# Optimization experiments

Hardware: AMD Instinct MI355X
Metric: run time of the kernel (lower is better)

The kernel has to match this reference:

```python
import jax, jax.numpy as jnp
import numpy as np

B, H, E = 32768, 1024, 512
VOCAB = 1600 * 20  # input_dim * 20


def setup_inputs() -> dict:
    key = jax.random.key(0)
    ks = jax.random.split(key, 13)
    sc_e = 1.0 / np.sqrt(E)
    sc_h = 1.0 / np.sqrt(H)
    sc_2h = 1.0 / np.sqrt(2 * H)
    # weights stored as [in, out] (transpose of torch Linear.weight)
    return {
        "s_t_minus_1": jax.random.normal(ks[0], (B, 1, H), jnp.float32),
        "y_t_minus_1": jax.random.randint(ks[1], (B, 1), 0, VOCAB, jnp.int64 if jax.config.jax_enable_x64 else jnp.int32),
        "c_t": jax.random.normal(ks[2], (B, 1, 2 * H), jnp.float32),
        "emb": jax.random.normal(ks[3], (VOCAB, E), jnp.float32),
        "Wz": jax.random.uniform(ks[4], (E, H), jnp.float32, -sc_e, sc_e),
        "Uz": jax.random.uniform(ks[5], (H, H), jnp.float32, -sc_h, sc_h),
        "Cz": jax.random.uniform(ks[6], (2 * H, H), jnp.float32, -sc_2h, sc_2h),
        "Wr": jax.random.uniform(ks[7], (E, H), jnp.float32, -sc_e, sc_e),
        "Ur": jax.random.uniform(ks[8], (H, H), jnp.float32, -sc_h, sc_h),
        "Cr": jax.random.uniform(ks[9], (2 * H, H), jnp.float32, -sc_2h, sc_2h),
        "W": jax.random.uniform(ks[10], (E, H), jnp.float32, -sc_e, sc_e),
        "U": jax.random.uniform(ks[11], (H, H), jnp.float32, -sc_h, sc_h),
        "C": jax.random.uniform(ks[12], (2 * H, H), jnp.float32, -sc_2h, sc_2h),
    }


def reference(s_t_minus_1, y_t_minus_1, c_t, emb, Wz, Uz, Cz, Wr, Ur, Cr, W, U, C):
    # embedding lookup: (B,1) -> (B,1,E)
    y = emb[y_t_minus_1]
    # gates, all contractions over last axis
    z_t = jax.nn.sigmoid(y @ Wz + s_t_minus_1 @ Uz + c_t @ Cz)  # (B,1,H)
    r_t = jax.nn.sigmoid(y @ Wr + s_t_minus_1 @ Ur + c_t @ Cr)  # (B,1,H)
    s_tilde = jnp.tanh(y @ W + (r_t * s_t_minus_1) @ U + c_t @ C)
    s_t = (1.0 - z_t) * s_t_minus_1 + z_t * s_tilde
    return s_t
```

## Files before the change

kernel.cpp:

```cpp
#include <hip/hip_runtime.h>

typedef unsigned short u16;
typedef float  f32x4  __attribute__((ext_vector_type(4)));
typedef short  bf16x8 __attribute__((ext_vector_type(8)));
typedef u16    u16x8  __attribute__((ext_vector_type(8)));

#define BROWS 32768
#define KTOT  3584
#define NKT   (KTOT / 64)

static __device__ __forceinline__ u16 f2b(float f) {
    unsigned x = __float_as_uint(f);
    x += 0x7fffu + ((x >> 16) & 1u);
    return (u16)(x >> 16);
}
static __device__ __forceinline__ float b2f(u16 u) {
    return __uint_as_float(((unsigned)u) << 16);
}
static __device__ __forceinline__ float sigm(float x) {
    return 1.f / (1.f + __expf(-x));
}
static __device__ __forceinline__ float tanh_s(float x) {
    float ax = fabsf(x);
    float e  = __expf(-2.f * ax);
    float t  = (1.f - e) / (1.f + e);
    return copysignf(t, x);
}
static __device__ __forceinline__ void gld16(const u16* g, u16* l) {
    __builtin_amdgcn_global_load_lds(
        (const __attribute__((address_space(1))) void*)g,
        (__attribute__((address_space(3))) void*)l, 16, 0, 0);
}

__global__ __launch_bounds__(256) void pack_x(
    const float* __restrict__ s, const int* __restrict__ y,
    const float* __restrict__ c, const float* __restrict__ emb,
    u16* __restrict__ X)
{
    long tid = (long)blockIdx.x * 256 + threadIdx.x;
    int  row = (int)(tid / 448);
    int  seg = (int)(tid % 448);
    int  e0  = seg * 8;
    const float* src;
    if (e0 < 512)        src = emb + (long)y[row] * 512 + e0;
    else if (e0 < 1536)  src = s   + (long)row * 1024 + (e0 - 512);
    else                 src = c   + (long)row * 2048 + (e0 - 1536);
    f32x4 a = *(const f32x4*)src;
    f32x4 b = *(const f32x4*)(src + 4);
    u16x8 o;
    o[0]=f2b(a[0]); o[1]=f2b(a[1]); o[2]=f2b(a[2]); o[3]=f2b(a[3]);
    o[4]=f2b(b[0]); o[5]=f2b(b[1]); o[6]=f2b(b[2]); o[7]=f2b(b[3]);
    *(u16x8*)&X[(long)row * KTOT + e0] = o;
}

__global__ __launch_bounds__(256) void wtrans_all(
    const float* __restrict__ Wz, const float* __restrict__ Uz,
    const float* __restrict__ Cz, const float* __restrict__ Wr,
    const float* __restrict__ Ur, const float* __restrict__ Cr,
    const float* __restrict__ W,  const float* __restrict__ U,
    const float* __restrict__ C,
    u16* __restrict__ WzrT, u16* __restrict__ W2T)
{
    __shared__ float t[32][33];
    int z = blockIdx.z;
    const float* src; u16* dst; int kd;
    switch (z) {
        case 0: src = Wz; dst = WzrT + 0;                  kd = 512;  break;
        case 1: src = Uz; dst = WzrT + 512;                kd = 1024; break;
        case 2: src = Cz; dst = WzrT + 1536;               kd = 2048; break;
        case 3: src = Wr; dst = WzrT + 1024 * KTOT;        kd = 512;  break;
        case 4: src = Ur; dst = WzrT + 1024 * KTOT + 512;  kd = 1024; break;
        case 5: src = Cr; dst = WzrT + 1024 * KTOT + 1536; kd = 2048; break;
        case 6: src = W;  dst = W2T + 0;                   kd = 512;  break;
        case 7: src = U;  dst = W2T + 512;                 kd = 1024; break;
        default: src = C; dst = W2T + 1536;                kd = 2048; break;
    }
    int k0 = blockIdx.x * 32;
    if (k0 >= kd) return;
    int n0 = blockIdx.y * 32;
    int tx = threadIdx.x, ty = threadIdx.y;
    #pragma unroll
    for (int r = ty; r < 32; r += 8)
        t[r][tx] = src[(long)(k0 + r) * 1024 + n0 + tx];
    __syncthreads();
    #pragma unroll
    for (int r = ty; r < 32; r += 8)
        dst[(long)(n0 + r) * KTOT + k0 + tx] = f2b(t[tx][r]);
}


#define RDA(P,m,ks)  a[m][ks]  = *(const bf16x8*)((P) + (m)*1024 + (ks)*512 + lane_off)
#define RDB(P,n,ks)  bb[n][ks] = *(const bf16x8*)((P) + (n)*1024 + (ks)*512 + lane_off)
#define RDA4(P,m0)   RDA(P,m0,0);RDA(P,m0,1);RDA(P,m0+1,0);RDA(P,m0+1,1);RDA(P,m0+2,0);RDA(P,m0+2,1);RDA(P,m0+3,0);RDA(P,m0+3,1)
#define RDB2(P,n0)   RDB(P,n0,0);RDB(P,n0,1);RDB(P,n0+1,0);RDB(P,n0+1,1)
#define MM1(m,n,ks) acc[m][n] = __builtin_amdgcn_mfma_f32_16x16x32_bf16(a[m][ks], bb[n][ks], acc[m][n], 0, 0, 0)
#define MMROW(m,n0) MM1(m,n0,0); MM1(m,n0,1); MM1(m,n0+1,0); MM1(m,n0+1,1)
#define MMQUAD(m0,n0) MMROW(m0,n0); MMROW(m0+1,n0); MMROW(m0+2,n0); MMROW(m0+3,n0)

#define PH_MID \
    __builtin_amdgcn_s_barrier(); \
    asm volatile("s_waitcnt lgkmcnt(0)" ::: "memory"); \
    __builtin_amdgcn_sched_barrier(0); \
    __builtin_amdgcn_s_setprio(1);

#define PH_END \
    __builtin_amdgcn_s_setprio(0); \
    __builtin_amdgcn_sched_barrier(0); \
    __builtin_amdgcn_s_barrier();

template<int MODE>
__global__ __launch_bounds__(512, 1) void gemm8(
    const u16* __restrict__ Xc, const u16* __restrict__ rsin,
    const u16* __restrict__ Wt,
    u16* __restrict__ zb, u16* __restrict__ rsb,
    const u16* __restrict__ zread, float* __restrict__ out, int NT)
{
    extern __shared__ u16 smem[];

    int bid = blockIdx.x, nwg = gridDim.x;
    int q   = nwg >> 3;
    int wg  = (bid & 7) * q + (bid >> 3);
    int bm  = wg / NT, bn = wg % NT;
    int R0  = bm * 256;
    int C0  = bn * 256;

    int t = threadIdx.x, w = t >> 6, l = t & 63;
    int wr = w >> 2, wc = w & 3;

    int rl   = l >> 2;
    int ccl  = ((l & 3) * 8) ^ ((l >> 5) * 16);
    int sr0  = w >> 1, sc = w & 1;
    int colb = sc * 32 + ccl;
    int offAx[2][2], offAr[2][2], offB[2][2];
    #pragma unroll
    for (int h = 0; h < 2; h++)
        #pragma unroll
        for (int i = 0; i < 2; i++) {
            int row = h * 128 + (sr0 + i * 4) * 16 + rl;
            offAx[h][i] = (R0 + row) * KTOT + colb;
            offAr[h][i] = (R0 + row) * 1024 + colb - 512;
            offB [h][i] = (C0 + row) * KTOT + colb;
        }

    auto stageA = [&](int kt) {
        int k0 = kt * 64;
        u16* Ld = smem + (kt & 1) * 32768;
        bool useR = (MODE == 1) && (k0 >= 512) && (k0 < 1536);
        #pragma unroll
        for (int h = 0; h < 2; h++)
            #pragma unroll
            for (int i = 0; i < 2; i++) {
                const u16* g = useR ? (rsin + (offAr[h][i] + k0))
                                    : (Xc   + (offAx[h][i] + k0));
                gld16(g, Ld + h * 8192 + (w + i * 8) * 512);
            }
    };
    auto stageB = [&](int kt) {
        int k0 = kt * 64;
        u16* Ld = smem + (kt & 1) * 32768 + 16384;
        #pragma unroll
        for (int h = 0; h < 2; h++)
            #pragma unroll
            for (int i = 0; i < 2; i++)
                gld16(Wt + (offB[h][i] + k0),
                      Ld + h * 8192 + (w + i * 8) * 512);
    };

    int lane_off = (l & 15) * 32 + (((l >> 4) * 8) ^ (((l >> 3) & 1) * 16));

    f32x4 acc[8][4];
    #pragma unroll
    for (int m = 0; m < 8; m++)
        #pragma unroll
        for (int n = 0; n < 4; n++)
            acc[m][n] = (f32x4){0.f, 0.f, 0.f, 0.f};

    bf16x8 a[8][2], bb[4][2];

    int aoff = wr * 8192;
    int boff = 16384 + (wc >> 1) * 8192 + (wc & 1) * 4096;

    stageA(0); stageB(0);
    stageA(1); stageB(1);
    asm volatile("s_waitcnt vmcnt(8)" ::: "memory");
    __builtin_amdgcn_s_barrier();
    {
        const u16* A0 = smem + aoff;
        const u16* B0 = smem + boff;
        RDA4(A0, 0); RDB2(B0, 0);
    }

    for (int kt = 0; kt < NKT; ++kt) {
        int bs = kt & 1;
        const u16* Ab = smem + bs * 32768 + aoff;
        const u16* Bb = smem + bs * 32768 + boff;
        const u16* An = smem + (bs ^ 1) * 32768 + aoff;
        const u16* Bn = smem + (bs ^ 1) * 32768 + boff;

        PH_MID; MMQUAD(0, 0); RDB2(Bb, 2); PH_END;
        PH_MID; MMQUAD(0, 2); RDA4(Ab, 4); PH_END;
        if (kt + 2 < NKT) stageB(kt + 2);
        PH_MID; MMQUAD(4, 2); PH_END;
        if (kt + 2 < NKT) {
            stageA(kt + 2);
            asm volatile("s_waitcnt vmcnt(8)" ::: "memory");
        } else {
            asm volatile("s_waitcnt vmcnt(0)" ::: "memory");
        }
        PH_MID; MMQUAD(4, 0);
        if (kt + 1 < NKT) { RDA4(An, 0); RDB2(Bn, 0); }
        PH_END;
    }

    int lr = (l >> 4) * 4, lc = l & 15;
    long R0w = R0 + wr * 128;
    int  C0w = C0 + wc * 64;
    if (MODE == 0) {
        if (C0 < 1024) {
            #pragma unroll
            for (int m = 0; m < 8; m++)
                #pragma unroll
                for (int n = 0; n < 4; n++) {
                    int col = C0w + n * 16 + lc;
                    #pragma unroll
                    for (int j = 0; j < 4; j++) {
                        long r = R0w + m * 16 + lr + j;
                        zb[r * 1024 + col] = f2b(sigm(acc[m][n][j]));
                    }
                }
        } else {
            #pragma unroll
            for (int m = 0; m < 8; m++)
                #pragma unroll
                for (int n = 0; n < 4; n++) {
                    int h = C0w + n * 16 + lc - 1024;
                    #pragma unroll
                    for (int j = 0; j < 4; j++) {
                        long r = R0w + m * 16 + lr + j;
                        float sv = b2f(Xc[r * KTOT + 512 + h]);
                        float rr = sigm(acc[m][n][j]);
                        rsb[r * 1024 + h] = f2b(rr * sv);
                    }
                }
        }
    } else {
        #pragma unroll
        for (int m = 0; m < 8; m++)
            #pragma unroll
            for (int n = 0; n < 4; n++) {
                int col = C0w + n * 16 + lc;
                #pragma unroll
                for (int j = 0; j < 4; j++) {
                    long r = R0w + m * 16 + lr + j;
                    float st = tanh_s(acc[m][n][j]);
                    float z  = b2f(zread[r * 1024 + col]);
                    float sv = b2f(Xc[r * KTOT + 512 + col]);
                    out[r * 1024 + col] = fmaf(z, st - sv, sv);
                }
            }
    }
}

extern "C" void kernel_launch(void* const* d_in, const int* in_sizes, int n_in,
                              void* d_out, int out_size, void* d_ws, size_t ws_size,
                              hipStream_t stream)
{
    const float* s   = (const float*)d_in[0];
    const int*   y   = (const int*)  d_in[1];
    const float* c   = (const float*)d_in[2];
    const float* emb = (const float*)d_in[3];
    const float* Wz  = (const float*)d_in[4];
    const float* Uz  = (const float*)d_in[5];
    const float* Cz  = (const float*)d_in[6];
    const float* Wr  = (const float*)d_in[7];
    const float* Ur  = (const float*)d_in[8];
    const float* Cr  = (const float*)d_in[9];
    const float* W   = (const float*)d_in[10];
    const float* U   = (const float*)d_in[11];
    const float* C   = (const float*)d_in[12];
    float* out = (float*)d_out;

    char* ws = (char*)d_ws;
    u16* Xcat = (u16*)(ws);
    u16* rsb  = (u16*)(ws + 234881024);
    u16* zbuf = (u16*)(ws + 301989888);
    u16* WzrT = (u16*)(ws + 369098752);
    u16* W2T  = (u16*)(ws + 383778816);

    hipFuncSetAttribute((const void*)gemm8<0>,
                        hipFuncAttributeMaxDynamicSharedMemorySize, 131072);
    hipFuncSetAttribute((const void*)gemm8<1>,
                        hipFuncAttributeMaxDynamicSharedMemorySize, 131072);

    pack_x<<<BROWS * 448 / 256, 256, 0, stream>>>(s, y, c, emb, Xcat);

    dim3 tb(32, 8);
    wtrans_all<<<dim3(64, 32, 9), tb, 0, stream>>>(
        Wz, Uz, Cz, Wr, Ur, Cr, W, U, C, WzrT, W2T);

    gemm8<0><<<(BROWS / 256) * (2048 / 256), 512, 131072, stream>>>(
        Xcat, nullptr, WzrT, zbuf, rsb, nullptr, nullptr, 2048 / 256);

    gemm8<1><<<(BROWS / 256) * (1024 / 256), 512, 131072, stream>>>(
        Xcat, rsb, W2T, nullptr, nullptr, zbuf, out, 1024 / 256);
}
```

Before: 803.8 us.

## Switch GEMM inner loop from 16x16x32 to 32x32x16 bf16 MFMA tiles

Replaces the 16x16x32 MFMA instruction with the 32x32x16 variant, reorganising the per-wave accumulators into 4x2 tiles of 32x32. LDS fragment reads and lane offsets are remapped to the new operand layout, and the epilogue indexing follows the 32x32 output layout. Larger MFMA tiles issue fewer instructions and fewer LDS reads per FLOP, which lowers LDS bandwidth pressure. The cost is a different register footprint and possible LDS bank conflicts with the existing swizzle.

```diff
diff --git a/kernel.cpp b/kernel.cpp
--- a/kernel.cpp
+++ b/kernel.cpp
@@ -1,9 +1,10 @@
 #include <hip/hip_runtime.h>
 
 typedef unsigned short u16;
-typedef float  f32x4  __attribute__((ext_vector_type(4)));
-typedef short  bf16x8 __attribute__((ext_vector_type(8)));
-typedef u16    u16x8  __attribute__((ext_vector_type(8)));
+typedef float  f32x4   __attribute__((ext_vector_type(4)));
+typedef float  f32x16  __attribute__((ext_vector_type(16)));
+typedef short  bf16x8  __attribute__((ext_vector_type(8)));
+typedef u16    u16x8   __attribute__((ext_vector_type(8)));
 
 #define BROWS 32768
 #define KTOT  3584
@@ -89,13 +90,14 @@
 }
 
 
-#define RDA(P,m,ks)  a[m][ks]  = *(const bf16x8*)((P) + (m)*1024 + (ks)*512 + lane_off)
-#define RDB(P,n,ks)  bb[n][ks] = *(const bf16x8*)((P) + (n)*1024 + (ks)*512 + lane_off)
-#define RDA4(P,m0)   RDA(P,m0,0);RDA(P,m0,1);RDA(P,m0+1,0);RDA(P,m0+1,1);RDA(P,m0+2,0);RDA(P,m0+2,1);RDA(P,m0+3,0);RDA(P,m0+3,1)
-#define RDB2(P,n0)   RDB(P,n0,0);RDB(P,n0,1);RDB(P,n0+1,0);RDB(P,n0+1,1)
-#define MM1(m,n,ks) acc[m][n] = __builtin_amdgcn_mfma_f32_16x16x32_bf16(a[m][ks], bb[n][ks], acc[m][n], 0, 0, 0)
-#define MMROW(m,n0) MM1(m,n0,0); MM1(m,n0,1); MM1(m,n0+1,0); MM1(m,n0+1,1)
-#define MMQUAD(m0,n0) MMROW(m0,n0); MMROW(m0+1,n0); MMROW(m0+2,n0); MMROW(m0+3,n0)
+#define RDA32(P,mt,ks) a[mt][ks] = *(const bf16x8*)((P) + (mt)*2048 + ((ks)>>1)*512 + (((ks)&1) ? laneX : laneO))
+#define RDB32(P,nt,ks) b[nt][ks] = *(const bf16x8*)((P) + (nt)*2048 + ((ks)>>1)*512 + (((ks)&1) ? laneX : laneO))
+#define RDA_T(P,mt) RDA32(P,mt,0); RDA32(P,mt,1); RDA32(P,mt,2); RDA32(P,mt,3)
+#define RDB_T(P,nt) RDB32(P,nt,0); RDB32(P,nt,1); RDB32(P,nt,2); RDB32(P,nt,3)
+#define MM32(mt,nt,ks) acc[mt][nt] = __builtin_amdgcn_mfma_f32_32x32x16_bf16(a[mt][ks], b[nt][ks], acc[mt][nt], 0, 0, 0)
+#define MMQ32(m0,m1,nt) \
+    MM32(m0,nt,0); MM32(m1,nt,0); MM32(m0,nt,1); MM32(m1,nt,1); \
+    MM32(m0,nt,2); MM32(m1,nt,2); MM32(m0,nt,3); MM32(m1,nt,3)
 
 #define PH_MID \
     __builtin_amdgcn_s_barrier(); \
@@ -166,29 +168,31 @@
                       Ld + h * 8192 + (w + i * 8) * 512);
     };
 
-    int lane_off = (l & 15) * 32 + (((l >> 4) * 8) ^ (((l >> 3) & 1) * 16));
-
-    f32x4 acc[8][4];
+    int laneO = ((l >> 4) & 1) * 1024 + (l & 15) * 32
+              + (((l >> 5) * 8) ^ (((l >> 3) & 1) * 16));
+    int laneX = laneO ^ 16;
+
+    f32x16 acc[4][2];
     #pragma unroll
-    for (int m = 0; m < 8; m++)
-        #pragma unroll
-        for (int n = 0; n < 4; n++)
-            acc[m][n] = (f32x4){0.f, 0.f, 0.f, 0.f};
-
-    bf16x8 a[8][2], bb[4][2];
+    for (int mt = 0; mt < 4; mt++)
+        #pragma unroll
+        for (int nt = 0; nt < 2; nt++)
+            acc[mt][nt] = (f32x16)(0.f);
+
+    bf16x8 a[4][4], b[2][4];
 
     int aoff = wr * 8192;
-    int boff = 16384 + (wc >> 1) * 8192 + (wc & 1) * 4096;
+    int boff = 16384 + wc * 4096;
+    const u16* Ae = smem + aoff;
+    const u16* Be = smem + boff;
+    const u16* Ao = Ae + 32768;
+    const u16* Bo = Be + 32768;
 
     stageA(0); stageB(0);
     stageA(1); stageB(1);
     asm volatile("s_waitcnt vmcnt(8)" ::: "memory");
     __builtin_amdgcn_s_barrier();
-    {
-        const u16* A0 = smem + aoff;
-        const u16* B0 = smem + boff;
-        RDA4(A0, 0); RDB2(B0, 0);
-    }
+    RDA_T(Ae, 0); RDA_T(Ae, 1); RDB_T(Be, 0);
 
     for (int kt = 0; kt < NKT; ++kt) {
         int bs = kt & 1;
@@ -197,66 +201,72 @@
         const u16* An = smem + (bs ^ 1) * 32768 + aoff;
         const u16* Bn = smem + (bs ^ 1) * 32768 + boff;
 
-        PH_MID; MMQUAD(0, 0); RDB2(Bb, 2); PH_END;
-        PH_MID; MMQUAD(0, 2); RDA4(Ab, 4); PH_END;
+        PH_MID; MMQ32(0, 1, 0); RDB_T(Bb, 1); PH_END;
+        PH_MID; MMQ32(0, 1, 1); RDA_T(Ab, 2); RDA_T(Ab, 3); PH_END;
         if (kt + 2 < NKT) stageB(kt + 2);
-        PH_MID; MMQUAD(4, 2); PH_END;
+        PH_MID; MMQ32(2, 3, 1); PH_END;
         if (kt + 2 < NKT) {
             stageA(kt + 2);
             asm volatile("s_waitcnt vmcnt(8)" ::: "memory");
         } else {
             asm volatile("s_waitcnt vmcnt(0)" ::: "memory");
         }
-        PH_MID; MMQUAD(4, 0);
-        if (kt + 1 < NKT) { RDA4(An, 0); RDB2(Bn, 0); }
+        PH_MID; MMQ32(2, 3, 0);
+        if (kt + 1 < NKT) { RDA_T(An, 0); RDA_T(An, 1); RDB_T(Bn, 0); }
         PH_END;
     }
 
-    int lr = (l >> 4) * 4, lc = l & 15;
+    int hi4 = (l >> 5) * 4, lc32 = l & 31;
     long R0w = R0 + wr * 128;
     int  C0w = C0 + wc * 64;
     if (MODE == 0) {
         if (C0 < 1024) {
             #pragma unroll
-            for (int m = 0; m < 8; m++)
+            for (int mt = 0; mt < 4; mt++)
                 #pragma unroll
-                for (int n = 0; n < 4; n++) {
-                    int col = C0w + n * 16 + lc;
+                for (int nt = 0; nt < 2; nt++) {
+                    int col = C0w + nt * 32 + lc32;
                     #pragma unroll
-                    for (int j = 0; j < 4; j++) {
-                        long r = R0w + m * 16 + lr + j;
-                        zb[r * 1024 + col] = f2b(sigm(acc[m][n][j]));
-                    }
+                    for (int qq = 0; qq < 4; qq++)
+                        #pragma unroll
+                        for (int jj = 0; jj < 4; jj++) {
+                            long r = R0w + mt * 32 + qq * 8 + hi4 + jj;
+                            zb[r * 1024 + col] = f2b(sigm(acc[mt][nt][qq * 4 + jj]));
+                        }
                 }
         } else {
             #pragma unroll
-            for (int m = 0; m < 8; m++)
+            for (int mt = 0; mt < 4; mt++)
                 #pragma unroll
-                for (int n = 0; n < 4; n++) {
-                    int h = C0w + n * 16 + lc - 1024;
+                for (int nt = 0; nt < 2; nt++) {
+                    int h = C0w + nt * 32 + lc32 - 1024;
                     #pragma unroll
-                    for (int j = 0; j < 4; j++) {
-                        long r = R0w + m * 16 + lr + j;
-                        float sv = b2f(Xc[r * KTOT + 512 + h]);
-                        float rr = sigm(acc[m][n][j]);
-                        rsb[r * 1024 + h] = f2b(rr * sv);
-                    }
+                    for (int qq = 0; qq < 4; qq++)
+                        #pragma unroll
+                        for (int jj = 0; jj < 4; jj++) {
+                            long r = R0w + mt * 32 + qq * 8 + hi4 + jj;
+                            float sv = b2f(Xc[r * KTOT + 512 + h]);
+                            float rr = sigm(acc[mt][nt][qq * 4 + jj]);
+                            rsb[r * 1024 + h] = f2b(rr * sv);
+                        }
                 }
         }
     } else {
         #pragma unroll
-        for (int m = 0; m < 8; m++)
-            #pragma unroll
-            for (int n = 0; n < 4; n++) {
-                int col = C0w + n * 16 + lc;
+        for (int mt = 0; mt < 4; mt++)
+            #pragma unroll
+            for (int nt = 0; nt < 2; nt++) {
+                int col = C0w + nt * 32 + lc32;
                 #pragma unroll
-                for (int j = 0; j < 4; j++) {
-                    long r = R0w + m * 16 + lr + j;
-                    float st = tanh_s(acc[m][n][j]);
-                    float z  = b2f(zread[r * 1024 + col]);
-                    float sv = b2f(Xc[r * KTOT + 512 + col]);
-                    out[r * 1024 + col] = fmaf(z, st - sv, sv);
-                }
+                for (int qq = 0; qq < 4; qq++)
+                    #pragma unroll
+                    for (int jj = 0; jj < 4; jj++) {
+                        long r = R0w + mt * 32 + qq * 8 + hi4 + jj;
+                        float st = tanh_s(acc[mt][nt][qq * 4 + jj]);
+                        float z  = b2f(zread[r * 1024 + col]);
+                        float sv = b2f(Xc[r * KTOT + 512 + col]);
+                        out[r * 1024 + col] = fmaf(z, st - sv, sv);
+                    }
             }
     }
 }
```

Result: slower. 863.2 us (+7.4%).
